# Kernel optimization log

Measured on AMD Instinct MI355X. Metric: run time of the kernel, lower is better.

The kernel has to match this reference:

```python
import jax, jax.numpy as jnp
import numpy as np

N = 50000      # nodes
E = 600000     # edges
D_IN = 5
D_H = 128
EPS = 1e-5     # BatchNorm1d default eps


def batch_norm(x, gamma, beta):
    # training-mode BN over the node dimension (biased variance)
    m = jnp.mean(x, axis=0)
    v = jnp.var(x, axis=0)
    return (x - m) * jax.lax.rsqrt(v + EPS) * gamma + beta


def gcn_conv(x, W, b, src, dst, w):
    # PyG GCNConv: linear transform, add self-loops (weight 1),
    # symmetric normalization D^-1/2 A D^-1/2, scatter-add to dst, + bias.
    x = x @ W                                   # [N, out]
    n = x.shape[0]
    loop = jnp.arange(n)
    src = jnp.concatenate([src, loop])
    dst = jnp.concatenate([dst, loop])
    w = jnp.concatenate([w, jnp.ones((n,), w.dtype)])
    deg = jax.ops.segment_sum(w, dst, num_segments=n)
    dis = jnp.where(deg > 0, jax.lax.rsqrt(jnp.maximum(deg, 1e-12)), 0.0)
    norm = dis[src] * w * dis[dst]              # [E+N]
    msgs = norm[:, None] * x[src]               # gather + scale
    return jax.ops.segment_sum(msgs, dst, num_segments=n) + b


def setup_inputs() -> dict:
    key = jax.random.key(0)
    ks = jax.random.split(key, 20)
    s_in = 1.0 / np.sqrt(D_IN)
    s_h = 1.0 / np.sqrt(D_H)
    return {
        "h": jax.random.normal(ks[0], (N, D_IN), jnp.float32),
        "edge_index": jax.random.randint(ks[1], (2, E), 0, N),
        "edge_weight": jax.random.uniform(ks[2], (E,), jnp.float32),
        "g0": 1.0 + 0.1 * jax.random.normal(ks[3], (D_IN,), jnp.float32),
        "be0": 0.1 * jax.random.normal(ks[4], (D_IN,), jnp.float32),
        "W1": jax.random.normal(ks[5], (D_IN, D_H), jnp.float32) * s_in,
        "b1": jax.random.normal(ks[6], (D_H,), jnp.float32) * s_in,
        "g1": 1.0 + 0.1 * jax.random.normal(ks[7], (D_H,), jnp.float32),
        "be1": 0.1 * jax.random.normal(ks[8], (D_H,), jnp.float32),
        "W2": jax.random.normal(ks[9], (D_H, D_H), jnp.float32) * s_h,
        "b2": jax.random.normal(ks[10], (D_H,), jnp.float32) * s_h,
        "g2": 1.0 + 0.1 * jax.random.normal(ks[11], (D_H,), jnp.float32),
        "be2": 0.1 * jax.random.normal(ks[12], (D_H,), jnp.float32),
        "Wmu": jax.random.normal(ks[13], (D_H, D_H), jnp.float32) * s_h,
        "bmu": jax.random.normal(ks[14], (D_H,), jnp.float32) * s_h,
        "Wls": jax.random.normal(ks[15], (D_H, D_H), jnp.float32) * s_h,
        "bls": jax.random.normal(ks[16], (D_H,), jnp.float32) * s_h,
    }


def reference(h, edge_index, edge_weight, g0, be0, W1, b1, g1, be1,
              W2, b2, g2, be2, Wmu, bmu, Wls, bls):
    src, dst = edge_index[0], edge_index[1]
    h = batch_norm(h, g0, be0)
    h = jax.nn.relu(batch_norm(gcn_conv(h, W1, b1, src, dst, edge_weight), g1, be1))
    # dropout p=0.1 treated as eval-mode (identity)
    h = jax.nn.relu(batch_norm(gcn_conv(h, W2, b2, src, dst, edge_weight), g2, be2))
    mu = h @ Wmu + bmu
    log_std = h @ Wls + bls
    return (mu, log_std)
```

## Files before the change

### kernel.cpp

```cpp
#include <hip/hip_runtime.h>

#define N_NODES 50000
#define N_EDGES 600000
#define D_IN 5
#define D_H 128
#define BN_EPS 1e-5f
#define SCAN_BLOCKS ((N_NODES + 255) / 256)
#define DEG_BLOCKS ((N_EDGES + 255) / 256)
#define FIX_SCALE 16777216.0f
#define FIX_INV   (1.0f / 16777216.0f)

typedef __bf16 bf16x8 __attribute__((ext_vector_type(8)));
typedef float  f32x4  __attribute__((ext_vector_type(4)));

__device__ inline unsigned short f2bfb(float f) {
    unsigned u = __builtin_bit_cast(unsigned, f);
    unsigned r = u + 0x7fffu + ((u >> 16) & 1u);
    return (unsigned short)(r >> 16);
}
__device__ inline float bflo(unsigned u) { return __builtin_bit_cast(float, u << 16); }
__device__ inline float bfhi(unsigned u) { return __builtin_bit_cast(float, u & 0xffff0000u); }

__device__ inline void stage_b(const unsigned short* __restrict__ Bt,
                               uint4* __restrict__ lds, int t)
{
#pragma unroll
    for (int i = 0; i < 8; ++i) {
        int slot = i * 256 + t;
        int fid = slot >> 6;
        int l = slot & 63;
        int row = (fid >> 2) * 16 + (l & 15);
        int boff = ((l >> 4) * 16 + (fid & 3) * 64) >> 1;
        lds[slot] = *(const uint4*)(Bt + row * D_H + boff);
    }
}

__global__ __launch_bounds__(256) void k_prep(const float* __restrict__ W2,
                                              const float* __restrict__ Wmu,
                                              const float* __restrict__ Wls,
                                              unsigned short* __restrict__ T2,
                                              unsigned short* __restrict__ Tmu,
                                              unsigned short* __restrict__ Tls,
                                              const float* __restrict__ h,
                                              float* __restrict__ stats0,
                                              const int* __restrict__ dst,
                                              const float* __restrict__ w,
                                              unsigned long long* __restrict__ degcnt,
                                              int* __restrict__ rank)
{
    __shared__ float ss[D_IN], sq[D_IN];
    int b = blockIdx.x;
    int t = threadIdx.x;
    if (b < 192) {
        int mat = b >> 6;
        int idx = (b & 63) * 256 + t;
        const float* W = (mat == 0) ? W2 : (mat == 1) ? Wmu : Wls;
        unsigned short* T = (mat == 0) ? T2 : (mat == 1) ? Tmu : Tls;
        int k = idx >> 7, n = idx & 127;
        T[n * D_H + k] = f2bfb(W[idx]);
    } else if (b < 192 + SCAN_BLOCKS) {
        if (t < D_IN) { ss[t] = 0.f; sq[t] = 0.f; }
        __syncthreads();
        int node = (b - 192) * 256 + t;
        float v[D_IN];
#pragma unroll
        for (int f = 0; f < D_IN; ++f)
            v[f] = (node < N_NODES) ? h[node * D_IN + f] : 0.f;
        int lane = t & 63;
#pragma unroll
        for (int f = 0; f < D_IN; ++f) {
            float s = v[f], q = v[f] * v[f];
            for (int off = 32; off > 0; off >>= 1) {
                s += __shfl_down(s, off);
                q += __shfl_down(q, off);
            }
            if (lane == 0) { atomicAdd(&ss[f], s); atomicAdd(&sq[f], q); }
        }
        __syncthreads();
        if (t < D_IN) {
            atomicAdd(&stats0[t], ss[t]);
            atomicAdd(&stats0[D_IN + t], sq[t]);
        }
    } else {
        int e = (b - 192 - SCAN_BLOCKS) * 256 + t;
        if (e < N_EDGES) {
            int d = dst[e];
            unsigned long long fx = (unsigned long long)(w[e] * FIX_SCALE + 0.5f);
            unsigned long long old = atomicAdd(degcnt + d, (1ull << 40) | fx);
            rank[e] = (int)(old >> 40);
        }
    }
}

__global__ __launch_bounds__(256) void k_scan1(const unsigned long long* __restrict__ degcnt,
                                               float* __restrict__ dis,
                                               int* __restrict__ blocksums)
{
    __shared__ int sm[256];
    int t = threadIdx.x;
    int i = blockIdx.x * 256 + t;
    int c = 0;
    if (i < N_NODES) {
        unsigned long long v = degcnt[i];
        c = (int)(v >> 40);
        float deg = (float)(v & ((1ull << 40) - 1)) * FIX_INV;
        dis[i] = rsqrtf(deg + 1.0f);
    }
    sm[t] = c;
    __syncthreads();
    for (int off = 128; off > 0; off >>= 1) {
        if (t < off) sm[t] += sm[t + off];
        __syncthreads();
    }
    if (t == 0) blocksums[blockIdx.x] = sm[0];
}

__global__ __launch_bounds__(256) void k_scan3(const unsigned long long* __restrict__ degcnt,
                                               int* __restrict__ rowptr,
                                               const int* __restrict__ blocksums)
{
    __shared__ int sm[256];
    __shared__ int soff;
    int t = threadIdx.x;
    int bid = blockIdx.x;
    int pre = (t < bid) ? blocksums[t] : 0;
    sm[t] = pre;
    __syncthreads();
    for (int off = 128; off > 0; off >>= 1) {
        if (t < off) sm[t] += sm[t + off];
        __syncthreads();
    }
    if (t == 0) soff = sm[0];
    __syncthreads();
    int i = bid * 256 + t;
    int c = (i < N_NODES) ? (int)(degcnt[i] >> 40) : 0;
    sm[t] = c;
    __syncthreads();
    for (int off = 1; off < 256; off <<= 1) {
        int v = (t >= off) ? sm[t - off] : 0;
        __syncthreads();
        sm[t] += v;
        __syncthreads();
    }
    if (i < N_NODES)
        rowptr[i] = soff + sm[t] - c;
    if (bid == 0 && t == 0)
        rowptr[N_NODES] = N_EDGES;
}

__global__ __launch_bounds__(256) void k_fill(const int* __restrict__ src,
                                              const int* __restrict__ dst,
                                              const float* __restrict__ w,
                                              const float* __restrict__ dis,
                                              const int* __restrict__ rowptr,
                                              const int* __restrict__ rank,
                                              int2* __restrict__ csr)
{
    int e = blockIdx.x * blockDim.x + threadIdx.x;
    if (e < N_EDGES) {
        int s = src[e], d = dst[e];
        float pn = dis[s] * w[e];
        int pos = rowptr[d] + rank[e];
        int2 pk;
        pk.x = s;
        pk.y = __builtin_bit_cast(int, pn);
        csr[pos] = pk;
    }
}

__global__ __launch_bounds__(256) void k_agg0(const float* __restrict__ h,
                                              const float* __restrict__ stats,
                                              const float* __restrict__ g0,
                                              const float* __restrict__ be0,
                                              const int* __restrict__ rowptr,
                                              const int2* __restrict__ csr,
                                              const float* __restrict__ dis,
                                              float* __restrict__ agg,
                                              float* __restrict__ statsA)
{
    __shared__ float sA[20];
    int t = threadIdx.x;
    if (t < 20) sA[t] = 0.f;
    __syncthreads();
    int n = blockIdx.x * 256 + t;
    float av[D_IN] = {0.f, 0.f, 0.f, 0.f, 0.f};
    if (n < N_NODES) {
        float sc[D_IN], sh[D_IN];
#pragma unroll
        for (int f = 0; f < D_IN; ++f) {
            float m = stats[f] * (1.0f / N_NODES);
            float var = stats[D_IN + f] * (1.0f / N_NODES) - m * m;
            sc[f] = rsqrtf(var + BN_EPS) * g0[f];
            sh[f] = be0[f] - m * sc[f];
        }
        float dn = dis[n];
        float acc[D_IN];
#pragma unroll
        for (int f = 0; f < D_IN; ++f)
            acc[f] = dn * (h[n * D_IN + f] * sc[f] + sh[f]);
        int e0 = rowptr[n], e1 = rowptr[n + 1];
        for (int e = e0; e < e1; ++e) {
            int2 pk = csr[e];
            int s = pk.x;
            float pn = __builtin_bit_cast(float, pk.y);
#pragma unroll
            for (int f = 0; f < D_IN; ++f)
                acc[f] += pn * (h[s * D_IN + f] * sc[f] + sh[f]);
        }
#pragma unroll
        for (int f = 0; f < D_IN; ++f) {
            float o = dn * acc[f];
            agg[n * D_IN + f] = o;
            av[f] = o;
        }
    }
    float red[20];
#pragma unroll
    for (int f = 0; f < D_IN; ++f) red[f] = av[f];
    {
        int idx = D_IN;
#pragma unroll
        for (int k = 0; k < D_IN; ++k)
#pragma unroll
            for (int l = k; l < D_IN; ++l)
                red[idx++] = av[k] * av[l];
    }
#pragma unroll
    for (int off = 32; off > 0; off >>= 1) {
#pragma unroll
        for (int i = 0; i < 20; ++i)
            red[i] += __shfl_down(red[i], off);
    }
    if ((t & 63) == 0) {
#pragma unroll
        for (int i = 0; i < 20; ++i)
            atomicAdd(&sA[i], red[i]);
    }
    __syncthreads();
    if (t < 20) atomicAdd(statsA + t, sA[t]);
}

__global__ __launch_bounds__(256) void k_l1(const float* __restrict__ agg,
                                            const float* __restrict__ W1,
                                            const float* __restrict__ b1,
                                            const float* __restrict__ g1,
                                            const float* __restrict__ be1,
                                            const float* __restrict__ statsA,
                                            unsigned short* __restrict__ x)
{
    int t = threadIdx.x;
    int idx0 = blockIdx.x * 256 + t;
    int f0 = (idx0 & 63) * 2;
    float wa[D_IN], wb[D_IN];
#pragma unroll
    for (int k = 0; k < D_IN; ++k) {
        wa[k] = W1[k * D_H + f0];
        wb[k] = W1[k * D_H + f0 + 1];
    }
    float ba = b1[f0], bb = b1[f0 + 1];

    const float inv = 1.0f / N_NODES;
    float S1[D_IN];
#pragma unroll
    for (int k = 0; k < D_IN; ++k) S1[k] = statsA[k];
    float M[D_IN][D_IN];
    {
        int idx = D_IN;
#pragma unroll
        for (int k = 0; k < D_IN; ++k)
#pragma unroll
            for (int l = k; l < D_IN; ++l) {
                float v = statsA[idx++];
                M[k][l] = v;
                M[l][k] = v;
            }
    }
    float t1a = 0.f, t1b = 0.f, qa = 0.f, qb = 0.f;
#pragma unroll
    for (int k = 0; k < D_IN; ++k) { t1a += wa[k] * S1[k]; t1b += wb[k] * S1[k]; }
#pragma unroll
    for (int k = 0; k < D_IN; ++k) {
        float ra = 0.f, rb = 0.f;
#pragma unroll
        for (int l = 0; l < D_IN; ++l) { ra += M[k][l] * wa[l]; rb += M[k][l] * wb[l]; }
        qa += wa[k] * ra;
        qb += wb[k] * rb;
    }
    float ma = t1a * inv, mb = t1b * inv;
    float mua = ma + ba, mub = mb + bb;
    float vara = fmaxf(qa * inv - ma * ma, 0.f);
    float varb = fmaxf(qb * inv - mb * mb, 0.f);
    float sca = rsqrtf(vara + BN_EPS) * g1[f0];
    float scb = rsqrtf(varb + BN_EPS) * g1[f0 + 1];
    float sha = be1[f0] - mua * sca;
    float shb = be1[f0 + 1] - mub * scb;

    const int stride = 512 * 256;
    for (int idx = idx0; idx < N_NODES * 64; idx += stride) {
        int n = idx >> 6;
        const float* a = agg + n * D_IN;
        float v0 = ba, v1 = bb;
#pragma unroll
        for (int k = 0; k < D_IN; ++k) { v0 += wa[k] * a[k]; v1 += wb[k] * a[k]; }
        v0 = fmaxf(v0 * sca + sha, 0.f);
        v1 = fmaxf(v1 * scb + shb, 0.f);
        ((unsigned*)x)[idx] = (unsigned)f2bfb(v0) | ((unsigned)f2bfb(v1) << 16);
    }
}

__global__ __launch_bounds__(256) void k_agg128(const unsigned short* __restrict__ x,
                                                const int* __restrict__ rowptr,
                                                const int2* __restrict__ csr,
                                                const float* __restrict__ dis,
                                                unsigned short* __restrict__ outb)
{
    int t = threadIdx.x;
    int n = blockIdx.x * 16 + (t >> 4);
    int f0 = (t & 15) * 8;
    if (n >= N_NODES) return;
    float dn = dis[n];
    uint4 hv = *(const uint4*)(x + (size_t)n * D_H + f0);
    float a0 = dn * bflo(hv.x), a1 = dn * bfhi(hv.x);
    float a2 = dn * bflo(hv.y), a3 = dn * bfhi(hv.y);
    float a4 = dn * bflo(hv.z), a5 = dn * bfhi(hv.z);
    float a6 = dn * bflo(hv.w), a7 = dn * bfhi(hv.w);
    int e = rowptr[n], e1 = rowptr[n + 1];
    for (; e + 4 <= e1; e += 4) {
        int2 p0 = csr[e + 0], p1 = csr[e + 1], p2 = csr[e + 2], p3 = csr[e + 3];
        float w0 = __builtin_bit_cast(float, p0.y);
        float w1 = __builtin_bit_cast(float, p1.y);
        float w2 = __builtin_bit_cast(float, p2.y);
        float w3 = __builtin_bit_cast(float, p3.y);
        uint4 v0 = *(const uint4*)(x + (size_t)p0.x * D_H + f0);
        uint4 v1 = *(const uint4*)(x + (size_t)p1.x * D_H + f0);
        uint4 v2 = *(const uint4*)(x + (size_t)p2.x * D_H + f0);
        uint4 v3 = *(const uint4*)(x + (size_t)p3.x * D_H + f0);
        a0 += w0 * bflo(v0.x) + w1 * bflo(v1.x) + w2 * bflo(v2.x) + w3 * bflo(v3.x);
        a1 += w0 * bfhi(v0.x) + w1 * bfhi(v1.x) + w2 * bfhi(v2.x) + w3 * bfhi(v3.x);
        a2 += w0 * bflo(v0.y) + w1 * bflo(v1.y) + w2 * bflo(v2.y) + w3 * bflo(v3.y);
        a3 += w0 * bfhi(v0.y) + w1 * bfhi(v1.y) + w2 * bfhi(v2.y) + w3 * bfhi(v3.y);
        a4 += w0 * bflo(v0.z) + w1 * bflo(v1.z) + w2 * bflo(v2.z) + w3 * bflo(v3.z);
        a5 += w0 * bfhi(v0.z) + w1 * bfhi(v1.z) + w2 * bfhi(v2.z) + w3 * bfhi(v3.z);
        a6 += w0 * bflo(v0.w) + w1 * bflo(v1.w) + w2 * bflo(v2.w) + w3 * bflo(v3.w);
        a7 += w0 * bfhi(v0.w) + w1 * bfhi(v1.w) + w2 * bfhi(v2.w) + w3 * bfhi(v3.w);
    }
    for (; e < e1; ++e) {
        int2 pk = csr[e];
        float pn = __builtin_bit_cast(float, pk.y);
        uint4 v = *(const uint4*)(x + (size_t)pk.x * D_H + f0);
        a0 += pn * bflo(v.x); a1 += pn * bfhi(v.x);
        a2 += pn * bflo(v.y); a3 += pn * bfhi(v.y);
        a4 += pn * bflo(v.z); a5 += pn * bfhi(v.z);
        a6 += pn * bflo(v.w); a7 += pn * bfhi(v.w);
    }
    uint4 o;
    o.x = (unsigned)f2bfb(dn * a0) | ((unsigned)f2bfb(dn * a1) << 16);
    o.y = (unsigned)f2bfb(dn * a2) | ((unsigned)f2bfb(dn * a3) << 16);
    o.z = (unsigned)f2bfb(dn * a4) | ((unsigned)f2bfb(dn * a5) << 16);
    o.w = (unsigned)f2bfb(dn * a6) | ((unsigned)f2bfb(dn * a7) << 16);
    *(uint4*)(outb + (size_t)n * D_H + f0) = o;
}

__global__ __launch_bounds__(256) void k_gemm_mf(const unsigned short* __restrict__ A,
                                                 const unsigned short* __restrict__ Bt,
                                                 const float* __restrict__ bias,
                                                 unsigned short* __restrict__ C,
                                                 float* __restrict__ stats)
{
    __shared__ uint4 ldsB[2048];
    __shared__ float sm_s[D_H], sm_q[D_H];
    int t = threadIdx.x;
    if (t < D_H) { sm_s[t] = 0.f; sm_q[t] = 0.f; }
    stage_b(Bt, ldsB, t);
    int wave = t >> 6, lane = t & 63;
    int m = lane & 15, quad = lane >> 4;
    int r0 = blockIdx.x * 64 + wave * 16;
    int arow = r0 + m < N_NODES ? r0 + m : N_NODES - 1;
    const bf16x8* ap = (const bf16x8*)(A + (size_t)arow * D_H + quad * 8);
    bf16x8 af[4];
#pragma unroll
    for (int ks = 0; ks < 4; ++ks) af[ks] = ap[ks * 4];
    __syncthreads();
    const bf16x8* bf = (const bf16x8*)ldsB;
    f32x4 acc[8];
#pragma unroll
    for (int ct = 0; ct < 8; ++ct) acc[ct] = (f32x4)(0.f);
#pragma unroll
    for (int ks = 0; ks < 4; ++ks) {
#pragma unroll
        for (int ct = 0; ct < 8; ++ct) {
            acc[ct] = __builtin_amdgcn_mfma_f32_16x16x32_bf16(
                af[ks], bf[(ct * 4 + ks) * 64 + lane], acc[ct], 0, 0, 0);
        }
    }
#pragma unroll
    for (int ct = 0; ct < 8; ++ct) {
        int col = ct * 16 + m;
        float bv = bias[col];
        float s = 0.f, q = 0.f;
#pragma unroll
        for (int r = 0; r < 4; ++r) {
            int rr = r0 + quad * 4 + r;
            if (rr < N_NODES) {
                float v = acc[ct][r] + bv;
                C[(size_t)rr * D_H + col] = f2bfb(v);
                s += v; q += v * v;
            }
        }
        atomicAdd(&sm_s[col], s);
        atomicAdd(&sm_q[col], q);
    }
    __syncthreads();
    if (t < D_H) {
        atomicAdd(stats + t, sm_s[t]);
        atomicAdd(stats + D_H + t, sm_q[t]);
    }
}

__global__ __launch_bounds__(256) void k_gemm_out_mf(const unsigned short* __restrict__ A,
                                                     const float* __restrict__ stats,
                                                     const float* __restrict__ g,
                                                     const float* __restrict__ be,
                                                     const unsigned short* __restrict__ Btmu,
                                                     const float* __restrict__ bmu,
                                                     const unsigned short* __restrict__ Btls,
                                                     const float* __restrict__ bls,
                                                     float* __restrict__ out)
{
    __shared__ uint4 ldsB[2048];
    int t = threadIdx.x;
    int wave = t >> 6, lane = t & 63;
    int m = lane & 15, quad = lane >> 4;
    int r0 = blockIdx.x * 64 + wave * 16;
    int arow = r0 + m < N_NODES ? r0 + m : N_NODES - 1;
    const unsigned short* arowp = A + (size_t)arow * D_H + quad * 8;
    const float inv = 1.0f / N_NODES;
    bf16x8 af[4];
#pragma unroll
    for (int ks = 0; ks < 4; ++ks) {
        uint4 av = *(const uint4*)(arowp + ks * 32);
        float vals[8] = { bflo(av.x), bfhi(av.x), bflo(av.y), bfhi(av.y),
                          bflo(av.z), bfhi(av.z), bflo(av.w), bfhi(av.w) };
        int fb = quad * 8 + ks * 32;
        unsigned short o[8];
#pragma unroll
        for (int j = 0; j < 8; ++j) {
            int f = fb + j;
            float mm = stats[f] * inv;
            float var = stats[D_H + f] * inv - mm * mm;
            float scv = rsqrtf(var + BN_EPS) * g[f];
            float shv = be[f] - mm * scv;
            o[j] = f2bfb(fmaxf(vals[j] * scv + shv, 0.f));
        }
        uint4 pk;
        pk.x = (unsigned)o[0] | ((unsigned)o[1] << 16);
        pk.y = (unsigned)o[2] | ((unsigned)o[3] << 16);
        pk.z = (unsigned)o[4] | ((unsigned)o[5] << 16);
        pk.w = (unsigned)o[6] | ((unsigned)o[7] << 16);
        af[ks] = __builtin_bit_cast(bf16x8, pk);
    }
    const bf16x8* bf = (const bf16x8*)ldsB;
#pragma unroll
    for (int half = 0; half < 2; ++half) {
        if (half) __syncthreads();
        stage_b(half ? Btls : Btmu, ldsB, t);
        __syncthreads();
        const float* bias = half ? bls : bmu;
        float* C = out + (half ? (size_t)N_NODES * D_H : 0);
        f32x4 acc[8];
#pragma unroll
        for (int ct = 0; ct < 8; ++ct) acc[ct] = (f32x4)(0.f);
#pragma unroll
        for (int ks = 0; ks < 4; ++ks) {
#pragma unroll
            for (int ct = 0; ct < 8; ++ct) {
                acc[ct] = __builtin_amdgcn_mfma_f32_16x16x32_bf16(
                    af[ks], bf[(ct * 4 + ks) * 64 + lane], acc[ct], 0, 0, 0);
            }
        }
#pragma unroll
        for (int ct = 0; ct < 8; ++ct) {
            int col = ct * 16 + m;
            float bv = bias[col];
#pragma unroll
            for (int r = 0; r < 4; ++r) {
                int rr = r0 + quad * 4 + r;
                if (rr < N_NODES)
                    C[(size_t)rr * D_H + col] = acc[ct][r] + bv;
            }
        }
    }
}

extern "C" void kernel_launch(void* const* d_in, const int* in_sizes, int n_in,
                              void* d_out, int out_size, void* d_ws, size_t ws_size,
                              hipStream_t stream)
{
    const float* h   = (const float*)d_in[0];
    const int*   eidx = (const int*)d_in[1];
    const float* ew  = (const float*)d_in[2];
    const float* g0  = (const float*)d_in[3];
    const float* be0 = (const float*)d_in[4];
    const float* W1  = (const float*)d_in[5];
    const float* b1  = (const float*)d_in[6];
    const float* g1  = (const float*)d_in[7];
    const float* be1 = (const float*)d_in[8];
    const float* W2  = (const float*)d_in[9];
    const float* b2  = (const float*)d_in[10];
    const float* g2  = (const float*)d_in[11];
    const float* be2 = (const float*)d_in[12];
    const float* Wmu = (const float*)d_in[13];
    const float* bmu = (const float*)d_in[14];
    const float* Wls = (const float*)d_in[15];
    const float* bls = (const float*)d_in[16];
    const int* srcv = eidx;
    const int* dstv = eidx + N_EDGES;
    float* out = (float*)d_out;

    char* ws = (char*)d_ws;
    size_t off = 0;
    auto alloc = [&](size_t bytes) -> char* {
        char* p = ws + off;
        off += (bytes + 255) & ~(size_t)255;
        return p;
    };
    float* stats0  = (float*)alloc(16 * 4);
    float* statsA  = (float*)alloc(32 * 4);
    float* stats2  = (float*)alloc(256 * 4);
    unsigned long long* degcnt = (unsigned long long*)alloc(N_NODES * 8);
    size_t zero_bytes = off;
    int*   rowptr  = (int*)  alloc((N_NODES + 1) * 4);
    float* dis     = (float*)alloc(N_NODES * 4);
    int*   rank    = (int*)  alloc((size_t)N_EDGES * 4);
    int*   blocksums = (int*)alloc(256 * 4);
    int2*  csr     = (int2*) alloc((size_t)N_EDGES * 8);
    float* agg0    = (float*)alloc(N_NODES * D_IN * 4);
    unsigned short* x1h  = (unsigned short*)alloc((size_t)N_NODES * D_H * 2);
    unsigned short* aggh = (unsigned short*)alloc((size_t)N_NODES * D_H * 2);
    unsigned short* c2h  = (unsigned short*)alloc((size_t)N_NODES * D_H * 2);
    unsigned short* Wt2   = (unsigned short*)alloc(D_H * D_H * 2);
    unsigned short* Wtmu  = (unsigned short*)alloc(D_H * D_H * 2);
    unsigned short* Wtls  = (unsigned short*)alloc(D_H * D_H * 2);
    (void)ws_size; (void)in_sizes; (void)n_in; (void)out_size;

    hipMemsetAsync(d_ws, 0, zero_bytes, stream);

    k_prep<<<192 + SCAN_BLOCKS + DEG_BLOCKS, 256, 0, stream>>>(
        W2, Wmu, Wls, Wt2, Wtmu, Wtls, h, stats0, dstv, ew, degcnt, rank);
    k_scan1<<<SCAN_BLOCKS, 256, 0, stream>>>(degcnt, dis, blocksums);
    k_scan3<<<SCAN_BLOCKS, 256, 0, stream>>>(degcnt, rowptr, blocksums);
    k_fill<<<DEG_BLOCKS, 256, 0, stream>>>(srcv, dstv, ew, dis, rowptr, rank, csr);
    k_agg0<<<SCAN_BLOCKS, 256, 0, stream>>>(h, stats0, g0, be0, rowptr, csr, dis,
                                            agg0, statsA);
    k_l1<<<512, 256, 0, stream>>>(agg0, W1, b1, g1, be1, statsA, x1h);
    k_agg128<<<(N_NODES + 15) / 16, 256, 0, stream>>>(x1h, rowptr, csr, dis, aggh);
    k_gemm_mf<<<(N_NODES + 63) / 64, 256, 0, stream>>>(aggh, Wt2, b2, c2h, stats2);
    k_gemm_out_mf<<<(N_NODES + 63) / 64, 256, 0, stream>>>(c2h, stats2, g2, be2,
                                                           Wtmu, bmu, Wtls, bls, out);
}
```

Measured before the change: 262.7 us.

## Fuse layer-2 aggregation into MFMA GEMM and pre-swizzle weights into fragment layout

Merges the 128-wide neighbor aggregation with the following MFMA GEMM. Each block aggregates its 64 rows into swizzled LDS and feeds them straight to the matrix cores, so the bf16 intermediate no longer makes a round trip through global memory and one launch is dropped. Weight matrices are now written by the prep kernel directly in MFMA fragment order, so both GEMM kernels read B fragments from global or L2 instead of staging them through LDS. The cost is lower parallelism for the gather phase: 64-node blocks with four sequential passes per thread instead of 16-node blocks. B fragments are also re-read from global memory by every wave.

Result: slower. 269.8 us (+2.7%).

```diff
diff --git a/kernel.cpp b/kernel.cpp
--- a/kernel.cpp
+++ b/kernel.cpp
@@ -20,20 +20,6 @@
 }
 __device__ inline float bflo(unsigned u) { return __builtin_bit_cast(float, u << 16); }
 __device__ inline float bfhi(unsigned u) { return __builtin_bit_cast(float, u & 0xffff0000u); }
-
-__device__ inline void stage_b(const unsigned short* __restrict__ Bt,
-                               uint4* __restrict__ lds, int t)
-{
-#pragma unroll
-    for (int i = 0; i < 8; ++i) {
-        int slot = i * 256 + t;
-        int fid = slot >> 6;
-        int l = slot & 63;
-        int row = (fid >> 2) * 16 + (l & 15);
-        int boff = ((l >> 4) * 16 + (fid & 3) * 64) >> 1;
-        lds[slot] = *(const uint4*)(Bt + row * D_H + boff);
-    }
-}
 
 __global__ __launch_bounds__(256) void k_prep(const float* __restrict__ W2,
                                               const float* __restrict__ Wmu,
@@ -57,7 +43,10 @@
         const float* W = (mat == 0) ? W2 : (mat == 1) ? Wmu : Wls;
         unsigned short* T = (mat == 0) ? T2 : (mat == 1) ? Tmu : Tls;
         int k = idx >> 7, n = idx & 127;
-        T[n * D_H + k] = f2bfb(W[idx]);
+        int fid = (n >> 4) * 4 + (k >> 5);
+        int l   = ((k >> 3) & 3) * 16 + (n & 15);
+        int j   = k & 7;
+        T[fid * 512 + l * 8 + j] = f2bfb(W[idx]);
     } else if (b < 192 + SCAN_BLOCKS) {
         if (t < D_IN) { ss[t] = 0.f; sq[t] = 0.f; }
         __syncthreads();
@@ -308,80 +297,85 @@
     }
 }
 
-__global__ __launch_bounds__(256) void k_agg128(const unsigned short* __restrict__ x,
+__global__ __launch_bounds__(256) void k_fused2(const unsigned short* __restrict__ x,
                                                 const int* __restrict__ rowptr,
                                                 const int2* __restrict__ csr,
                                                 const float* __restrict__ dis,
-                                                unsigned short* __restrict__ outb)
-{
-    int t = threadIdx.x;
-    int n = blockIdx.x * 16 + (t >> 4);
-    int f0 = (t & 15) * 8;
-    if (n >= N_NODES) return;
-    float dn = dis[n];
-    uint4 hv = *(const uint4*)(x + (size_t)n * D_H + f0);
-    float a0 = dn * bflo(hv.x), a1 = dn * bfhi(hv.x);
-    float a2 = dn * bflo(hv.y), a3 = dn * bfhi(hv.y);
-    float a4 = dn * bflo(hv.z), a5 = dn * bfhi(hv.z);
-    float a6 = dn * bflo(hv.w), a7 = dn * bfhi(hv.w);
-    int e = rowptr[n], e1 = rowptr[n + 1];
-    for (; e + 4 <= e1; e += 4) {
-        int2 p0 = csr[e + 0], p1 = csr[e + 1], p2 = csr[e + 2], p3 = csr[e + 3];
-        float w0 = __builtin_bit_cast(float, p0.y);
-        float w1 = __builtin_bit_cast(float, p1.y);
-        float w2 = __builtin_bit_cast(float, p2.y);
-        float w3 = __builtin_bit_cast(float, p3.y);
-        uint4 v0 = *(const uint4*)(x + (size_t)p0.x * D_H + f0);
-        uint4 v1 = *(const uint4*)(x + (size_t)p1.x * D_H + f0);
-        uint4 v2 = *(const uint4*)(x + (size_t)p2.x * D_H + f0);
-        uint4 v3 = *(const uint4*)(x + (size_t)p3.x * D_H + f0);
-        a0 += w0 * bflo(v0.x) + w1 * bflo(v1.x) + w2 * bflo(v2.x) + w3 * bflo(v3.x);
-        a1 += w0 * bfhi(v0.x) + w1 * bfhi(v1.x) + w2 * bfhi(v2.x) + w3 * bfhi(v3.x);
-        a2 += w0 * bflo(v0.y) + w1 * bflo(v1.y) + w2 * bflo(v2.y) + w3 * bflo(v3.y);
-        a3 += w0 * bfhi(v0.y) + w1 * bfhi(v1.y) + w2 * bfhi(v2.y) + w3 * bfhi(v3.y);
-        a4 += w0 * bflo(v0.z) + w1 * bflo(v1.z) + w2 * bflo(v2.z) + w3 * bflo(v3.z);
-        a5 += w0 * bfhi(v0.z) + w1 * bfhi(v1.z) + w2 * bfhi(v2.z) + w3 * bfhi(v3.z);
-        a6 += w0 * bflo(v0.w) + w1 * bflo(v1.w) + w2 * bflo(v2.w) + w3 * bflo(v3.w);
-        a7 += w0 * bfhi(v0.w) + w1 * bfhi(v1.w) + w2 * bfhi(v2.w) + w3 * bfhi(v3.w);
-    }
-    for (; e < e1; ++e) {
-        int2 pk = csr[e];
-        float pn = __builtin_bit_cast(float, pk.y);
-        uint4 v = *(const uint4*)(x + (size_t)pk.x * D_H + f0);
-        a0 += pn * bflo(v.x); a1 += pn * bfhi(v.x);
-        a2 += pn * bflo(v.y); a3 += pn * bfhi(v.y);
-        a4 += pn * bflo(v.z); a5 += pn * bfhi(v.z);
-        a6 += pn * bflo(v.w); a7 += pn * bfhi(v.w);
-    }
-    uint4 o;
-    o.x = (unsigned)f2bfb(dn * a0) | ((unsigned)f2bfb(dn * a1) << 16);
-    o.y = (unsigned)f2bfb(dn * a2) | ((unsigned)f2bfb(dn * a3) << 16);
-    o.z = (unsigned)f2bfb(dn * a4) | ((unsigned)f2bfb(dn * a5) << 16);
-    o.w = (unsigned)f2bfb(dn * a6) | ((unsigned)f2bfb(dn * a7) << 16);
-    *(uint4*)(outb + (size_t)n * D_H + f0) = o;
-}
-
-__global__ __launch_bounds__(256) void k_gemm_mf(const unsigned short* __restrict__ A,
-                                                 const unsigned short* __restrict__ Bt,
-                                                 const float* __restrict__ bias,
-                                                 unsigned short* __restrict__ C,
-                                                 float* __restrict__ stats)
-{
-    __shared__ uint4 ldsB[2048];
+                                                const unsigned short* __restrict__ Bf,
+                                                const float* __restrict__ bias,
+                                                unsigned short* __restrict__ C,
+                                                float* __restrict__ stats)
+{
+    __shared__ uint4 ldsA[1024];
     __shared__ float sm_s[D_H], sm_q[D_H];
     int t = threadIdx.x;
     if (t < D_H) { sm_s[t] = 0.f; sm_q[t] = 0.f; }
-    stage_b(Bt, ldsB, t);
+    int m_ = t >> 4;
+    int fc = t & 15;
+    int f0 = fc * 8;
+    int ksw = fc >> 2, quadw = fc & 3;
+    int sbase = ksw * 64 + quadw * 16 + m_;
+    int gsw = ksw * 2 + (quadw & 1);
+
+    for (int p = 0; p < 4; ++p) {
+        int n = blockIdx.x * 64 + p * 16 + m_;
+        uint4 o = {0u, 0u, 0u, 0u};
+        if (n < N_NODES) {
+            float dn = dis[n];
+            uint4 hv = *(const uint4*)(x + (size_t)n * D_H + f0);
+            float a0 = dn * bflo(hv.x), a1 = dn * bfhi(hv.x);
+            float a2 = dn * bflo(hv.y), a3 = dn * bfhi(hv.y);
+            float a4 = dn * bflo(hv.z), a5 = dn * bfhi(hv.z);
+            float a6 = dn * bflo(hv.w), a7 = dn * bfhi(hv.w);
+            int e = rowptr[n], e1 = rowptr[n + 1];
+            for (; e + 4 <= e1; e += 4) {
+                int2 p0 = csr[e + 0], p1 = csr[e + 1], p2 = csr[e + 2], p3 = csr[e + 3];
+                float w0 = __builtin_bit_cast(float, p0.y);
+                float w1 = __builtin_bit_cast(float, p1.y);
+                float w2 = __builtin_bit_cast(float, p2.y);
+                float w3 = __builtin_bit_cast(float, p3.y);
+                uint4 v0 = *(const uint4*)(x + (size_t)p0.x * D_H + f0);
+                uint4 v1 = *(const uint4*)(x + (size_t)p1.x * D_H + f0);
+                uint4 v2 = *(const uint4*)(x + (size_t)p2.x * D_H + f0);
+                uint4 v3 = *(const uint4*)(x + (size_t)p3.x * D_H + f0);
+                a0 += w0 * bflo(v0.x) + w1 * bflo(v1.x) + w2 * bflo(v2.x) + w3 * bflo(v3.x);
+                a1 += w0 * bfhi(v0.x) + w1 * bfhi(v1.x) + w2 * bfhi(v2.x) + w3 * bfhi(v3.x);
+                a2 += w0 * bflo(v0.y) + w1 * bflo(v1.y) + w2 * bflo(v2.y) + w3 * bflo(v3.y);
+                a3 += w0 * bfhi(v0.y) + w1 * bfhi(v1.y) + w2 * bfhi(v2.y) + w3 * bfhi(v3.y);
+                a4 += w0 * bflo(v0.z) + w1 * bflo(v1.z) + w2 * bflo(v2.z) + w3 * bflo(v3.z);
+                a5 += w0 * bfhi(v0.z) + w1 * bfhi(v1.z) + w2 * bfhi(v2.z) + w3 * bfhi(v3.z);
+                a6 += w0 * bflo(v0.w) + w1 * bflo(v1.w) + w2 * bflo(v2.w) + w3 * bflo(v3.w);
+                a7 += w0 * bfhi(v0.w) + w1 * bfhi(v1.w) + w2 * bfhi(v2.w) + w3 * bfhi(v3.w);
+            }
+            for (; e < e1; ++e) {
+                int2 pk = csr[e];
+                float pn = __builtin_bit_cast(float, pk.y);
+                uint4 v = *(const uint4*)(x + (size_t)pk.x * D_H + f0);
+                a0 += pn * bflo(v.x); a1 += pn * bfhi(v.x);
+                a2 += pn * bflo(v.y); a3 += pn * bfhi(v.y);
+                a4 += pn * bflo(v.z); a5 += pn * bfhi(v.z);
+                a6 += pn * bflo(v.w); a7 += pn * bfhi(v.w);
+            }
+            o.x = (unsigned)f2bfb(dn * a0) | ((unsigned)f2bfb(dn * a1) << 16);
+            o.y = (unsigned)f2bfb(dn * a2) | ((unsigned)f2bfb(dn * a3) << 16);
+            o.z = (unsigned)f2bfb(dn * a4) | ((unsigned)f2bfb(dn * a5) << 16);
+            o.w = (unsigned)f2bfb(dn * a6) | ((unsigned)f2bfb(dn * a7) << 16);
+        }
+        ldsA[(p * 256 + sbase) ^ gsw] = o;
+    }
+    __syncthreads();
+
     int wave = t >> 6, lane = t & 63;
     int m = lane & 15, quad = lane >> 4;
     int r0 = blockIdx.x * 64 + wave * 16;
-    int arow = r0 + m < N_NODES ? r0 + m : N_NODES - 1;
-    const bf16x8* ap = (const bf16x8*)(A + (size_t)arow * D_H + quad * 8);
     bf16x8 af[4];
 #pragma unroll
-    for (int ks = 0; ks < 4; ++ks) af[ks] = ap[ks * 4];
-    __syncthreads();
-    const bf16x8* bf = (const bf16x8*)ldsB;
+    for (int ks = 0; ks < 4; ++ks) {
+        int s = (wave * 4 + ks) * 64 + lane;
+        int g = ks * 2 + (quad & 1);
+        af[ks] = ((const bf16x8*)ldsA)[s ^ g];
+    }
+    const bf16x8* bp = (const bf16x8*)Bf;
     f32x4 acc[8];
 #pragma unroll
     for (int ct = 0; ct < 8; ++ct) acc[ct] = (f32x4)(0.f);
@@ -390,7 +384,7 @@
 #pragma unroll
         for (int ct = 0; ct < 8; ++ct) {
             acc[ct] = __builtin_amdgcn_mfma_f32_16x16x32_bf16(
-                af[ks], bf[(ct * 4 + ks) * 64 + lane], acc[ct], 0, 0, 0);
+                af[ks], bp[(ct * 4 + ks) * 64 + lane], acc[ct], 0, 0, 0);
         }
     }
 #pragma unroll
@@ -421,13 +415,12 @@
                                                      const float* __restrict__ stats,
                                                      const float* __restrict__ g,
                                                      const float* __restrict__ be,
-                                                     const unsigned short* __restrict__ Btmu,
+                                                     const unsigned short* __restrict__ Bfmu,
                                                      const float* __restrict__ bmu,
-                                                     const unsigned short* __restrict__ Btls,
+                                                     const unsigned short* __restrict__ Bfls,
                                                      const float* __restrict__ bls,
                                                      float* __restrict__ out)
 {
-    __shared__ uint4 ldsB[2048];
     int t = threadIdx.x;
     int wave = t >> 6, lane = t & 63;
     int m = lane & 15, quad = lane >> 4;
@@ -459,12 +452,9 @@
         pk.w = (unsigned)o[6] | ((unsigned)o[7] << 16);
         af[ks] = __builtin_bit_cast(bf16x8, pk);
     }
-    const bf16x8* bf = (const bf16x8*)ldsB;
 #pragma unroll
     for (int half = 0; half < 2; ++half) {
-        if (half) __syncthreads();
-        stage_b(half ? Btls : Btmu, ldsB, t);
-        __syncthreads();
+        const bf16x8* bp = (const bf16x8*)(half ? Bfls : Bfmu);
         const float* bias = half ? bls : bmu;
         float* C = out + (half ? (size_t)N_NODES * D_H : 0);
         f32x4 acc[8];
@@ -475,7 +465,7 @@
 #pragma unroll
             for (int ct = 0; ct < 8; ++ct) {
                 acc[ct] = __builtin_amdgcn_mfma_f32_16x16x32_bf16(
-                    af[ks], bf[(ct * 4 + ks) * 64 + lane], acc[ct], 0, 0, 0);
+                    af[ks], bp[(ct * 4 + ks) * 64 + lane], acc[ct], 0, 0, 0);
             }
         }
 #pragma unroll
@@ -536,7 +526,6 @@
     int2*  csr     = (int2*) alloc((size_t)N_EDGES * 8);
     float* agg0    = (float*)alloc(N_NODES * D_IN * 4);
     unsigned short* x1h  = (unsigned short*)alloc((size_t)N_NODES * D_H * 2);
-    unsigned short* aggh = (unsigned short*)alloc((size_t)N_NODES * D_H * 2);
     unsigned short* c2h  = (unsigned short*)alloc((size_t)N_NODES * D_H * 2);
     unsigned short* Wt2   = (unsigned short*)alloc(D_H * D_H * 2);
     unsigned short* Wtmu  = (unsigned short*)alloc(D_H * D_H * 2);
@@ -553,8 +542,8 @@
     k_agg0<<<SCAN_BLOCKS, 256, 0, stream>>>(h, stats0, g0, be0, rowptr, csr, dis,
                                             agg0, statsA);
     k_l1<<<512, 256, 0, stream>>>(agg0, W1, b1, g1, be1, statsA, x1h);
-    k_agg128<<<(N_NODES + 15) / 16, 256, 0, stream>>>(x1h, rowptr, csr, dis, aggh);
-    k_gemm_mf<<<(N_NODES + 63) / 64, 256, 0, stream>>>(aggh, Wt2, b2, c2h, stats2);
+    k_fused2<<<(N_NODES + 63) / 64, 256, 0, stream>>>(x1h, rowptr, csr, dis,
+                                                      Wt2, b2, c2h, stats2);
     k_gemm_out_mf<<<(N_NODES + 63) / 64, 256, 0, stream>>>(c2h, stats2, g2, be2,
                                                            Wtmu, bmu, Wtls, bls, out);
 }
```

## Merge scan kernels via grid-wide atomic barrier and unroll aggregation by eight

Applied to the files above, without the earlier changes.

Fuses the two scan kernels into one. A global atomic counter acts as a grid barrier: each block publishes its block sum, spins until all 196 blocks have arrived, then computes its prefix offset. This removes one kernel launch, but it relies on all blocks being co-resident, which should hold for so few blocks. Separately, the 128-wide aggregation loop gains an 8-edge unrolled body, putting more gather loads in flight per iteration at the cost of extra registers.

Result: slower. 272.8 us (+3.8%).

```diff
diff --git a/kernel.cpp b/kernel.cpp
--- a/kernel.cpp
+++ b/kernel.cpp
@@ -92,13 +92,16 @@
     }
 }
 
-__global__ __launch_bounds__(256) void k_scan1(const unsigned long long* __restrict__ degcnt,
-                                               float* __restrict__ dis,
-                                               int* __restrict__ blocksums)
+__global__ __launch_bounds__(256) void k_scan(const unsigned long long* __restrict__ degcnt,
+                                              float* __restrict__ dis,
+                                              int* __restrict__ rowptr,
+                                              int* __restrict__ blocksums,
+                                              int* __restrict__ sync_ctr)
 {
     __shared__ int sm[256];
-    int t = threadIdx.x;
-    int i = blockIdx.x * 256 + t;
+    __shared__ int soff;
+    int t = threadIdx.x, bid = blockIdx.x;
+    int i = bid * 256 + t;
     int c = 0;
     if (i < N_NODES) {
         unsigned long long v = degcnt[i];
@@ -112,18 +115,17 @@
         if (t < off) sm[t] += sm[t + off];
         __syncthreads();
     }
-    if (t == 0) blocksums[blockIdx.x] = sm[0];
-}
-
-__global__ __launch_bounds__(256) void k_scan3(const unsigned long long* __restrict__ degcnt,
-                                               int* __restrict__ rowptr,
-                                               const int* __restrict__ blocksums)
-{
-    __shared__ int sm[256];
-    __shared__ int soff;
-    int t = threadIdx.x;
-    int bid = blockIdx.x;
-    int pre = (t < bid) ? blocksums[t] : 0;
+    if (t == 0) {
+        atomicExch(&blocksums[bid], sm[0]);
+        __threadfence();
+        atomicAdd(sync_ctr, 1);
+    }
+    if (t == 0) {
+        while (atomicAdd(sync_ctr, 0) < SCAN_BLOCKS)
+            __builtin_amdgcn_s_sleep(8);
+    }
+    __syncthreads();
+    int pre = (t < bid) ? atomicAdd(&blocksums[t], 0) : 0;
     sm[t] = pre;
     __syncthreads();
     for (int off = 128; off > 0; off >>= 1) {
@@ -132,8 +134,6 @@
     }
     if (t == 0) soff = sm[0];
     __syncthreads();
-    int i = bid * 256 + t;
-    int c = (i < N_NODES) ? (int)(degcnt[i] >> 40) : 0;
     sm[t] = c;
     __syncthreads();
     for (int off = 1; off < 256; off <<= 1) {
@@ -325,6 +325,38 @@
     float a4 = dn * bflo(hv.z), a5 = dn * bfhi(hv.z);
     float a6 = dn * bflo(hv.w), a7 = dn * bfhi(hv.w);
     int e = rowptr[n], e1 = rowptr[n + 1];
+    for (; e + 8 <= e1; e += 8) {
+        int2 p0 = csr[e + 0], p1 = csr[e + 1], p2 = csr[e + 2], p3 = csr[e + 3];
+        int2 p4 = csr[e + 4], p5 = csr[e + 5], p6 = csr[e + 6], p7 = csr[e + 7];
+        uint4 v0 = *(const uint4*)(x + (size_t)p0.x * D_H + f0);
+        uint4 v1 = *(const uint4*)(x + (size_t)p1.x * D_H + f0);
+        uint4 v2 = *(const uint4*)(x + (size_t)p2.x * D_H + f0);
+        uint4 v3 = *(const uint4*)(x + (size_t)p3.x * D_H + f0);
+        uint4 v4 = *(const uint4*)(x + (size_t)p4.x * D_H + f0);
+        uint4 v5 = *(const uint4*)(x + (size_t)p5.x * D_H + f0);
+        uint4 v6 = *(const uint4*)(x + (size_t)p6.x * D_H + f0);
+        uint4 v7 = *(const uint4*)(x + (size_t)p7.x * D_H + f0);
+        float w0 = __builtin_bit_cast(float, p0.y), w1 = __builtin_bit_cast(float, p1.y);
+        float w2 = __builtin_bit_cast(float, p2.y), w3 = __builtin_bit_cast(float, p3.y);
+        float w4 = __builtin_bit_cast(float, p4.y), w5 = __builtin_bit_cast(float, p5.y);
+        float w6 = __builtin_bit_cast(float, p6.y), w7 = __builtin_bit_cast(float, p7.y);
+        a0 += w0 * bflo(v0.x) + w1 * bflo(v1.x) + w2 * bflo(v2.x) + w3 * bflo(v3.x)
+            + w4 * bflo(v4.x) + w5 * bflo(v5.x) + w6 * bflo(v6.x) + w7 * bflo(v7.x);
+        a1 += w0 * bfhi(v0.x) + w1 * bfhi(v1.x) + w2 * bfhi(v2.x) + w3 * bfhi(v3.x)
+            + w4 * bfhi(v4.x) + w5 * bfhi(v5.x) + w6 * bfhi(v6.x) + w7 * bfhi(v7.x);
+        a2 += w0 * bflo(v0.y) + w1 * bflo(v1.y) + w2 * bflo(v2.y) + w3 * bflo(v3.y)
+            + w4 * bflo(v4.y) + w5 * bflo(v5.y) + w6 * bflo(v6.y) + w7 * bflo(v7.y);
+        a3 += w0 * bfhi(v0.y) + w1 * bfhi(v1.y) + w2 * bfhi(v2.y) + w3 * bfhi(v3.y)
+            + w4 * bfhi(v4.y) + w5 * bfhi(v5.y) + w6 * bfhi(v6.y) + w7 * bfhi(v7.y);
+        a4 += w0 * bflo(v0.z) + w1 * bflo(v1.z) + w2 * bflo(v2.z) + w3 * bflo(v3.z)
+            + w4 * bflo(v4.z) + w5 * bflo(v5.z) + w6 * bflo(v6.z) + w7 * bflo(v7.z);
+        a5 += w0 * bfhi(v0.z) + w1 * bfhi(v1.z) + w2 * bfhi(v2.z) + w3 * bfhi(v3.z)
+            + w4 * bfhi(v4.z) + w5 * bfhi(v5.z) + w6 * bfhi(v6.z) + w7 * bfhi(v7.z);
+        a6 += w0 * bflo(v0.w) + w1 * bflo(v1.w) + w2 * bflo(v2.w) + w3 * bflo(v3.w)
+            + w4 * bflo(v4.w) + w5 * bflo(v5.w) + w6 * bflo(v6.w) + w7 * bflo(v7.w);
+        a7 += w0 * bfhi(v0.w) + w1 * bfhi(v1.w) + w2 * bfhi(v2.w) + w3 * bfhi(v3.w)
+            + w4 * bfhi(v4.w) + w5 * bfhi(v5.w) + w6 * bfhi(v6.w) + w7 * bfhi(v7.w);
+    }
     for (; e + 4 <= e1; e += 4) {
         int2 p0 = csr[e + 0], p1 = csr[e + 1], p2 = csr[e + 2], p3 = csr[e + 3];
         float w0 = __builtin_bit_cast(float, p0.y);
@@ -527,6 +559,7 @@
     float* stats0  = (float*)alloc(16 * 4);
     float* statsA  = (float*)alloc(32 * 4);
     float* stats2  = (float*)alloc(256 * 4);
+    int*   sync_ctr = (int*)alloc(256);
     unsigned long long* degcnt = (unsigned long long*)alloc(N_NODES * 8);
     size_t zero_bytes = off;
     int*   rowptr  = (int*)  alloc((N_NODES + 1) * 4);
@@ -547,8 +580,7 @@
 
     k_prep<<<192 + SCAN_BLOCKS + DEG_BLOCKS, 256, 0, stream>>>(
         W2, Wmu, Wls, Wt2, Wtmu, Wtls, h, stats0, dstv, ew, degcnt, rank);
-    k_scan1<<<SCAN_BLOCKS, 256, 0, stream>>>(degcnt, dis, blocksums);
-    k_scan3<<<SCAN_BLOCKS, 256, 0, stream>>>(degcnt, rowptr, blocksums);
+    k_scan<<<SCAN_BLOCKS, 256, 0, stream>>>(degcnt, dis, rowptr, blocksums, sync_ctr);
     k_fill<<<DEG_BLOCKS, 256, 0, stream>>>(srcv, dstv, ew, dis, rowptr, rank, csr);
     k_agg0<<<SCAN_BLOCKS, 256, 0, stream>>>(h, stats0, g0, be0, rowptr, csr, dis,
                                             agg0, statsA);
```

## Split 128-wide neighbor aggregation into four 32-feature passes with deeper unroll

Applied to the files above, without the earlier changes.

Replaces the single full-width aggregation kernel with four launches, each covering one 32-feature slice, with four threads per node instead of sixteen. Each pass gathers only 64 bytes per neighbor row, so its working set of the 12.8 MB bf16 feature matrix is a quarter the size and may fit in cache. The edge loop is unrolled to 8 to keep more gathers in flight. In exchange, the CSR and rowptr arrays are re-read four times, three extra kernel launches are added, and each gather is a narrower per-row access.

New measurement: 292.8 us. 11.5% more time.

```diff
diff --git a/kernel.cpp b/kernel.cpp
--- a/kernel.cpp
+++ b/kernel.cpp
@@ -7,6 +7,7 @@
 #define BN_EPS 1e-5f
 #define SCAN_BLOCKS ((N_NODES + 255) / 256)
 #define DEG_BLOCKS ((N_EDGES + 255) / 256)
+#define AGG32_BLOCKS ((N_NODES + 63) / 64)
 #define FIX_SCALE 16777216.0f
 #define FIX_INV   (1.0f / 16777216.0f)
 
@@ -308,16 +309,17 @@
     }
 }
 
-__global__ __launch_bounds__(256) void k_agg128(const unsigned short* __restrict__ x,
-                                                const int* __restrict__ rowptr,
-                                                const int2* __restrict__ csr,
-                                                const float* __restrict__ dis,
-                                                unsigned short* __restrict__ outb)
-{
-    int t = threadIdx.x;
-    int n = blockIdx.x * 16 + (t >> 4);
-    int f0 = (t & 15) * 8;
+__global__ __launch_bounds__(256) void k_agg32(const unsigned short* __restrict__ x,
+                                               const int* __restrict__ rowptr,
+                                               const int2* __restrict__ csr,
+                                               const float* __restrict__ dis,
+                                               unsigned short* __restrict__ outb,
+                                               int fq)
+{
+    int t = threadIdx.x;
+    int n = blockIdx.x * 64 + (t >> 2);
     if (n >= N_NODES) return;
+    int f0 = fq * 32 + (t & 3) * 8;
     float dn = dis[n];
     uint4 hv = *(const uint4*)(x + (size_t)n * D_H + f0);
     float a0 = dn * bflo(hv.x), a1 = dn * bfhi(hv.x);
@@ -325,24 +327,37 @@
     float a4 = dn * bflo(hv.z), a5 = dn * bfhi(hv.z);
     float a6 = dn * bflo(hv.w), a7 = dn * bfhi(hv.w);
     int e = rowptr[n], e1 = rowptr[n + 1];
-    for (; e + 4 <= e1; e += 4) {
+    for (; e + 8 <= e1; e += 8) {
         int2 p0 = csr[e + 0], p1 = csr[e + 1], p2 = csr[e + 2], p3 = csr[e + 3];
-        float w0 = __builtin_bit_cast(float, p0.y);
-        float w1 = __builtin_bit_cast(float, p1.y);
-        float w2 = __builtin_bit_cast(float, p2.y);
-        float w3 = __builtin_bit_cast(float, p3.y);
+        int2 p4 = csr[e + 4], p5 = csr[e + 5], p6 = csr[e + 6], p7 = csr[e + 7];
         uint4 v0 = *(const uint4*)(x + (size_t)p0.x * D_H + f0);
         uint4 v1 = *(const uint4*)(x + (size_t)p1.x * D_H + f0);
         uint4 v2 = *(const uint4*)(x + (size_t)p2.x * D_H + f0);
         uint4 v3 = *(const uint4*)(x + (size_t)p3.x * D_H + f0);
-        a0 += w0 * bflo(v0.x) + w1 * bflo(v1.x) + w2 * bflo(v2.x) + w3 * bflo(v3.x);
-        a1 += w0 * bfhi(v0.x) + w1 * bfhi(v1.x) + w2 * bfhi(v2.x) + w3 * bfhi(v3.x);
-        a2 += w0 * bflo(v0.y) + w1 * bflo(v1.y) + w2 * bflo(v2.y) + w3 * bflo(v3.y);
-        a3 += w0 * bfhi(v0.y) + w1 * bfhi(v1.y) + w2 * bfhi(v2.y) + w3 * bfhi(v3.y);
-        a4 += w0 * bflo(v0.z) + w1 * bflo(v1.z) + w2 * bflo(v2.z) + w3 * bflo(v3.z);
-        a5 += w0 * bfhi(v0.z) + w1 * bfhi(v1.z) + w2 * bfhi(v2.z) + w3 * bfhi(v3.z);
-        a6 += w0 * bflo(v0.w) + w1 * bflo(v1.w) + w2 * bflo(v2.w) + w3 * bflo(v3.w);
-        a7 += w0 * bfhi(v0.w) + w1 * bfhi(v1.w) + w2 * bfhi(v2.w) + w3 * bfhi(v3.w);
+        uint4 v4 = *(const uint4*)(x + (size_t)p4.x * D_H + f0);
+        uint4 v5 = *(const uint4*)(x + (size_t)p5.x * D_H + f0);
+        uint4 v6 = *(const uint4*)(x + (size_t)p6.x * D_H + f0);
+        uint4 v7 = *(const uint4*)(x + (size_t)p7.x * D_H + f0);
+        float w0 = __builtin_bit_cast(float, p0.y), w1 = __builtin_bit_cast(float, p1.y);
+        float w2 = __builtin_bit_cast(float, p2.y), w3 = __builtin_bit_cast(float, p3.y);
+        float w4 = __builtin_bit_cast(float, p4.y), w5 = __builtin_bit_cast(float, p5.y);
+        float w6 = __builtin_bit_cast(float, p6.y), w7 = __builtin_bit_cast(float, p7.y);
+        a0 += w0 * bflo(v0.x) + w1 * bflo(v1.x) + w2 * bflo(v2.x) + w3 * bflo(v3.x)
+            + w4 * bflo(v4.x) + w5 * bflo(v5.x) + w6 * bflo(v6.x) + w7 * bflo(v7.x);
+        a1 += w0 * bfhi(v0.x) + w1 * bfhi(v1.x) + w2 * bfhi(v2.x) + w3 * bfhi(v3.x)
+            + w4 * bfhi(v4.x) + w5 * bfhi(v5.x) + w6 * bfhi(v6.x) + w7 * bfhi(v7.x);
+        a2 += w0 * bflo(v0.y) + w1 * bflo(v1.y) + w2 * bflo(v2.y) + w3 * bflo(v3.y)
+            + w4 * bflo(v4.y) + w5 * bflo(v5.y) + w6 * bflo(v6.y) + w7 * bflo(v7.y);
+        a3 += w0 * bfhi(v0.y) + w1 * bfhi(v1.y) + w2 * bfhi(v2.y) + w3 * bfhi(v3.y)
+            + w4 * bfhi(v4.y) + w5 * bfhi(v5.y) + w6 * bfhi(v6.y) + w7 * bfhi(v7.y);
+        a4 += w0 * bflo(v0.z) + w1 * bflo(v1.z) + w2 * bflo(v2.z) + w3 * bflo(v3.z)
+            + w4 * bflo(v4.z) + w5 * bflo(v5.z) + w6 * bflo(v6.z) + w7 * bflo(v7.z);
+        a5 += w0 * bfhi(v0.z) + w1 * bfhi(v1.z) + w2 * bfhi(v2.z) + w3 * bfhi(v3.z)
+            + w4 * bfhi(v4.z) + w5 * bfhi(v5.z) + w6 * bfhi(v6.z) + w7 * bfhi(v7.z);
+        a6 += w0 * bflo(v0.w) + w1 * bflo(v1.w) + w2 * bflo(v2.w) + w3 * bflo(v3.w)
+            + w4 * bflo(v4.w) + w5 * bflo(v5.w) + w6 * bflo(v6.w) + w7 * bflo(v7.w);
+        a7 += w0 * bfhi(v0.w) + w1 * bfhi(v1.w) + w2 * bfhi(v2.w) + w3 * bfhi(v3.w)
+            + w4 * bfhi(v4.w) + w5 * bfhi(v5.w) + w6 * bfhi(v6.w) + w7 * bfhi(v7.w);
     }
     for (; e < e1; ++e) {
         int2 pk = csr[e];
@@ -553,7 +568,10 @@
     k_agg0<<<SCAN_BLOCKS, 256, 0, stream>>>(h, stats0, g0, be0, rowptr, csr, dis,
                                             agg0, statsA);
     k_l1<<<512, 256, 0, stream>>>(agg0, W1, b1, g1, be1, statsA, x1h);
-    k_agg128<<<(N_NODES + 15) / 16, 256, 0, stream>>>(x1h, rowptr, csr, dis, aggh);
+    k_agg32<<<AGG32_BLOCKS, 256, 0, stream>>>(x1h, rowptr, csr, dis, aggh, 0);
+    k_agg32<<<AGG32_BLOCKS, 256, 0, stream>>>(x1h, rowptr, csr, dis, aggh, 1);
+    k_agg32<<<AGG32_BLOCKS, 256, 0, stream>>>(x1h, rowptr, csr, dis, aggh, 2);
+    k_agg32<<<AGG32_BLOCKS, 256, 0, stream>>>(x1h, rowptr, csr, dis, aggh, 3);
     k_gemm_mf<<<(N_NODES + 63) / 64, 256, 0, stream>>>(aggh, Wt2, b2, c2h, stats2);
     k_gemm_out_mf<<<(N_NODES + 63) / 64, 256, 0, stream>>>(c2h, stats2, g2, be2,
                                                            Wtmu, bmu, Wtls, bls, out);
```
